# Kernel optimization log

Measured on AMD Instinct MI355X. Metric: run time of the kernel, lower is better.

## Reference

```python
import jax, jax.numpy as jnp
import numpy as np

N_NODES = 50000
N_EDGES = 1_600_000
DIMS = [512, 256, 128]


def _edge_softmax(vals, rows, n):
    # sparse softmax over dim=1 (per source row), only over stored edges
    m = jax.ops.segment_max(vals, rows, num_segments=n)
    e = jnp.exp(vals - m[rows])
    s = jax.ops.segment_sum(e, rows, num_segments=n)
    return e / s[rows]


def _spmm(att, rows, cols, H, n):
    # (sparse C) @ H : gather source cols, scale by edge weight, scatter-add to rows
    return jax.ops.segment_sum(att[:, None] * H[cols], rows, num_segments=n)


def setup_inputs() -> dict:
    key = jax.random.key(0)
    ks = jax.random.split(key, 12)
    X = jax.random.normal(ks[0], (N_NODES, DIMS[0]), dtype=jnp.float32)
    edge_row = jax.random.randint(ks[1], (N_EDGES,), 0, N_NODES, dtype=jnp.int32)
    edge_col = jax.random.randint(ks[2], (N_EDGES,), 0, N_NODES, dtype=jnp.int32)
    A_vals = jnp.ones((N_EDGES,), dtype=jnp.float32)
    def lin(k, dout, din):
        lim = 1.0 / np.sqrt(din)
        return jax.random.uniform(k, (dout, din), jnp.float32, -lim, lim)
    W0 = lin(ks[3], DIMS[1], DIMS[0])
    b0 = jax.random.uniform(ks[4], (DIMS[1],), jnp.float32, -1/np.sqrt(DIMS[0]), 1/np.sqrt(DIMS[0]))
    W1 = lin(ks[5], DIMS[2], DIMS[1])
    b1 = jax.random.uniform(ks[6], (DIMS[2],), jnp.float32, -1/np.sqrt(DIMS[1]), 1/np.sqrt(DIMS[1]))
    v00 = jax.random.normal(ks[7], (DIMS[1],), dtype=jnp.float32)
    v01 = jax.random.normal(ks[8], (DIMS[1],), dtype=jnp.float32)
    v10 = jax.random.normal(ks[9], (DIMS[2],), dtype=jnp.float32)
    v11 = jax.random.normal(ks[10], (DIMS[2],), dtype=jnp.float32)
    return {"X": X, "edge_row": edge_row, "edge_col": edge_col, "A_vals": A_vals,
            "W0": W0, "b0": b0, "W1": W1, "b1": b1,
            "v00": v00, "v01": v01, "v10": v10, "v11": v11}


def reference(X, edge_row, edge_col, A_vals, W0, b0, W1, b1, v00, v01, v10, v11):
    n = X.shape[0]
    layers = [((W0, b0), (v00, v01)), ((W1, b1), (v10, v11))]
    H = X
    atts = []
    # encoder
    for (W, b), (va, vb) in layers:
        M = H @ W.T + b                               # [N, d_out]
        # attention logits are computed under no_grad in the original
        f1 = M @ va                                   # [N]
        f2 = M @ vb
        logits = jax.lax.stop_gradient(A_vals * (f1[edge_row] + f2[edge_col]))
        att = _edge_softmax(jax.nn.sigmoid(logits), edge_row, n)
        H = _spmm(att, edge_row, edge_col, M, n)
        atts.append(att)
    final_H = H
    # decoder (tied weights, reverse order, reuse encoder attention)
    for ((W, _), _), att in zip(reversed(layers), reversed(atts)):
        H = H @ W                                     # F.linear(H, W.t()) == H @ W
        H = _spmm(att, edge_row, edge_col, H, n)
    return H, final_H
```

## Files before the change

### kernel.cpp

```cpp
#include <hip/hip_runtime.h>
#include <cstdint>
#include <cstddef>

typedef __attribute__((ext_vector_type(8))) short bf16x8;
typedef __attribute__((ext_vector_type(4))) float f32x4;

__device__ __forceinline__ ushort f2b(float f) {
    union { float f; uint32_t u; } v; v.f = f;
    uint32_t r = (v.u + 0x7fffu + ((v.u >> 16) & 1u)) >> 16;
    return (ushort)r;
}
__device__ __forceinline__ float b2f(ushort b) {
    union { uint32_t u; float f; } v; v.u = ((uint32_t)b) << 16;
    return v.f;
}


__global__ __launch_bounds__(256) void hist_kernel(const int* __restrict__ rows,
                                                   int* __restrict__ bhist, int E, int nb) {
    __shared__ int h[512];
    for (int i = threadIdx.x; i < nb; i += 256) h[i] = 0;
    __syncthreads();
    int stride = gridDim.x * blockDim.x;
    for (int e = blockIdx.x * blockDim.x + threadIdx.x; e < E; e += stride)
        atomicAdd(&h[rows[e] >> 7], 1);
    __syncthreads();
    for (int i = threadIdx.x; i < nb; i += 256)
        if (h[i]) atomicAdd(&bhist[i], h[i]);
}

__global__ __launch_bounds__(512) void scan512(const int* __restrict__ bhist,
                                               int* __restrict__ boff, int* __restrict__ gcur,
                                               int* __restrict__ rp, int nb, int E, int N) {
    __shared__ int sm[512];
    int v = ((int)threadIdx.x < nb) ? bhist[threadIdx.x] : 0;
    sm[threadIdx.x] = v;
    __syncthreads();
    for (int off = 1; off < 512; off <<= 1) {
        int t = ((int)threadIdx.x >= off) ? sm[threadIdx.x - off] : 0;
        __syncthreads();
        sm[threadIdx.x] += t;
        __syncthreads();
    }
    if ((int)threadIdx.x < nb) {
        int e0 = sm[threadIdx.x] - v;
        boff[threadIdx.x] = e0;
        gcur[threadIdx.x] = e0;
    }
    if (threadIdx.x == 0) { boff[nb] = E; rp[N] = E; }
}

__global__ __launch_bounds__(256) void binpass(const int* __restrict__ rows,
                                               const int* __restrict__ cols,
                                               const float* __restrict__ avals,
                                               int* __restrict__ gcur,
                                               uint2* __restrict__ tmp, int E, int nb) {
    __shared__ int hist[512];
    __shared__ int base[512];
    int e0 = blockIdx.x * 4096;
    int nE = min(4096, E - e0);
    for (int i = threadIdx.x; i < nb; i += 256) hist[i] = 0;
    __syncthreads();
    for (int i = threadIdx.x; i < nE; i += 256)
        atomicAdd(&hist[rows[e0 + i] >> 7], 1);
    __syncthreads();
    for (int i = threadIdx.x; i < nb; i += 256) {
        int c = hist[i];
        if (c) base[i] = atomicAdd(&gcur[i], c);
        hist[i] = 0;
    }
    __syncthreads();
    for (int i = threadIdx.x; i < nE; i += 256) {
        int r = rows[e0 + i];
        int b = r >> 7;
        int loc = atomicAdd(&hist[b], 1);
        uint2 t;
        t.x = ((uint32_t)r << 16) | (uint32_t)cols[e0 + i];
        t.y = __float_as_uint(avals[e0 + i]);
        tmp[base[b] + loc] = t;
    }
}

__global__ __launch_bounds__(256) void bucketpass(const uint2* __restrict__ tmp,
                                                  const int* __restrict__ boff,
                                                  int* __restrict__ rp,
                                                  int* __restrict__ col_s,
                                                  float* __restrict__ a_s, int N) {
    __shared__ int cnt[128];
    __shared__ int pre[128];
    int b = blockIdx.x;
    int r0 = b << 7;
    int nr = min(128, N - r0);
    int t0 = boff[b], t1 = boff[b + 1];
    if ((int)threadIdx.x < 128) cnt[threadIdx.x] = 0;
    __syncthreads();
    for (int i = t0 + (int)threadIdx.x; i < t1; i += 256)
        atomicAdd(&cnt[(tmp[i].x >> 16) - r0], 1);
    __syncthreads();
    if ((int)threadIdx.x < 128) pre[threadIdx.x] = cnt[threadIdx.x];
    __syncthreads();
    for (int off = 1; off < 128; off <<= 1) {
        int t = ((int)threadIdx.x >= off && (int)threadIdx.x < 128) ? pre[threadIdx.x - off] : 0;
        __syncthreads();
        if ((int)threadIdx.x < 128) pre[threadIdx.x] += t;
        __syncthreads();
    }
    if ((int)threadIdx.x < nr) {
        int ex = pre[threadIdx.x] - cnt[threadIdx.x];
        rp[r0 + threadIdx.x] = t0 + ex;
        cnt[threadIdx.x] = t0 + ex;
    }
    __syncthreads();
    for (int i = t0 + (int)threadIdx.x; i < t1; i += 256) {
        uint2 t = tmp[i];
        int lr = (int)(t.x >> 16) - r0;
        int pos = atomicAdd(&cnt[lr], 1);
        col_s[pos] = (int)(t.x & 0xffffu);
        a_s[pos] = __uint_as_float(t.y);
    }
}

__global__ void f2b4_kernel(const float* __restrict__ src, ushort* __restrict__ dst, int n4) {
    int i = blockIdx.x * blockDim.x + threadIdx.x;
    if (i < n4) {
        float4 v = ((const float4*)src)[i];
        ushort4 o;
        o.x = f2b(v.x); o.y = f2b(v.y); o.z = f2b(v.z); o.w = f2b(v.w);
        ((ushort4*)dst)[i] = o;
    }
}

__global__ void transpose_f2b_kernel(const float* __restrict__ W, ushort* __restrict__ Wt,
                                     int rows, int cols) {
    int idx = blockIdx.x * blockDim.x + threadIdx.x;
    if (idx < rows * cols) {
        int r = idx / cols, c = idx % cols;
        Wt[(size_t)c * rows + r] = f2b(W[idx]);
    }
}

__global__ __launch_bounds__(256) void gemm_bf16(const ushort* __restrict__ A,
                                                 const ushort* __restrict__ B,
                                                 const float* __restrict__ bias,
                                                 float* __restrict__ Cf,
                                                 ushort* __restrict__ Ch,
                                                 int M, int K, int Dout) {
    __shared__ ushort As[128][40];
    __shared__ ushort Bs[128][40];
    int bm = blockIdx.y * 128, bn = blockIdx.x * 128;
    int tid = threadIdx.x;
    int w = tid >> 6, l = tid & 63;
    int wm = (w & 1) * 64, wn = (w >> 1) * 64;
    int lm = l & 15, quad = l >> 4;

    f32x4 acc[4][4] = {};

    for (int k0 = 0; k0 < K; k0 += 32) {
#pragma unroll
        for (int it = 0; it < 2; ++it) {
            int L = tid + it * 256;
            int row = L >> 2;
            int ch = (L & 3) * 8;
            int ga = bm + row; if (ga > M - 1) ga = M - 1;
            *(uint4*)&As[row][ch] = *(const uint4*)(A + (size_t)ga * K + k0 + ch);
            *(uint4*)&Bs[row][ch] = *(const uint4*)(B + (size_t)(bn + row) * K + k0 + ch);
        }
        __syncthreads();
        bf16x8 af[4], bfr[4];
#pragma unroll
        for (int i = 0; i < 4; ++i) af[i]  = *(const bf16x8*)&As[wm + i * 16 + lm][quad * 8];
#pragma unroll
        for (int j = 0; j < 4; ++j) bfr[j] = *(const bf16x8*)&Bs[wn + j * 16 + lm][quad * 8];
#pragma unroll
        for (int i = 0; i < 4; ++i)
#pragma unroll
            for (int j = 0; j < 4; ++j)
                acc[i][j] = __builtin_amdgcn_mfma_f32_16x16x32_bf16(af[i], bfr[j], acc[i][j], 0, 0, 0);
        __syncthreads();
    }

    float bv[4] = {0.f, 0.f, 0.f, 0.f};
    if (bias) {
#pragma unroll
        for (int j = 0; j < 4; ++j) bv[j] = bias[bn + wn + j * 16 + lm];
    }
#pragma unroll
    for (int i = 0; i < 4; ++i) {
#pragma unroll
        for (int r = 0; r < 4; ++r) {
            int row = bm + wm + i * 16 + quad * 4 + r;
            if (row < M) {
#pragma unroll
                for (int j = 0; j < 4; ++j) {
                    int col = bn + wn + j * 16 + lm;
                    float v = acc[i][j][r] + bv[j];
                    if (Cf) Cf[(size_t)row * Dout + col] = v;
                    if (Ch) Ch[(size_t)row * Dout + col] = f2b(v);
                }
            }
        }
    }
}

__global__ void fvec_bf16(const ushort* __restrict__ Mh, const float* __restrict__ va,
                          const float* __restrict__ vb, float* __restrict__ f1,
                          float* __restrict__ f2, int d) {
    int n = blockIdx.x;
    int lane = threadIdx.x;
    const ushort* row = Mh + (size_t)n * d;
    float s1 = 0.f, s2 = 0.f;
    for (int k = lane; k < d; k += 64) {
        float m = b2f(row[k]);
        s1 += m * va[k];
        s2 += m * vb[k];
    }
#pragma unroll
    for (int off = 32; off > 0; off >>= 1) {
        s1 += __shfl_xor(s1, off);
        s2 += __shfl_xor(s2, off);
    }
    if (lane == 0) { f1[n] = s1; f2[n] = s2; }
}

__global__ void att_kernel(const int* __restrict__ rp, const int* __restrict__ col_s,
                           const float* __restrict__ a_s, const float* __restrict__ f1,
                           const float* __restrict__ f2, float* __restrict__ att) {
    int r = blockIdx.x;
    int lane = threadIdx.x;
    int beg = rp[r], end = rp[r + 1];
    if (beg == end) return;
    float fr = f1[r];
    float m = -1e30f;
    for (int j = beg + lane; j < end; j += 64) {
        float x = a_s[j] * (fr + f2[col_s[j]]);
        float v = 1.f / (1.f + __expf(-x));
        att[j] = v;
        m = fmaxf(m, v);
    }
#pragma unroll
    for (int off = 32; off > 0; off >>= 1) m = fmaxf(m, __shfl_xor(m, off));
    float s = 0.f;
    for (int j = beg + lane; j < end; j += 64) {
        float e = __expf(att[j] - m);
        att[j] = e;
        s += e;
    }
#pragma unroll
    for (int off = 32; off > 0; off >>= 1) s += __shfl_xor(s, off);
    float inv = 1.f / s;
    for (int j = beg + lane; j < end; j += 64) att[j] *= inv;
}

__global__ __launch_bounds__(256) void spmm_bf16(const int* __restrict__ rp,
                                                 const int* __restrict__ col_s,
                                                 const float* __restrict__ att,
                                                 const ushort* __restrict__ H,
                                                 const float* __restrict__ bias,
                                                 ushort* __restrict__ Oh,
                                                 float* __restrict__ Of,
                                                 int d4, int N) {
    int tid = threadIdx.x;
    int rpb = 256 / d4;
    int r = blockIdx.x * rpb + tid / d4;
    int lane = tid % d4;
    if (r >= N) return;
    int beg = rp[r], end = rp[r + 1];
    float4 acc = make_float4(0.f, 0.f, 0.f, 0.f);
    const ushort4* H4 = (const ushort4*)H;
    int j = beg;
    for (; j + 4 <= end; j += 4) {
        int c0 = col_s[j], c1 = col_s[j + 1], c2 = col_s[j + 2], c3 = col_s[j + 3];
        float w0 = att[j], w1 = att[j + 1], w2 = att[j + 2], w3 = att[j + 3];
        ushort4 h0 = H4[(size_t)c0 * d4 + lane];
        ushort4 h1 = H4[(size_t)c1 * d4 + lane];
        ushort4 h2 = H4[(size_t)c2 * d4 + lane];
        ushort4 h3 = H4[(size_t)c3 * d4 + lane];
        acc.x += w0 * b2f(h0.x) + w1 * b2f(h1.x) + w2 * b2f(h2.x) + w3 * b2f(h3.x);
        acc.y += w0 * b2f(h0.y) + w1 * b2f(h1.y) + w2 * b2f(h2.y) + w3 * b2f(h3.y);
        acc.z += w0 * b2f(h0.z) + w1 * b2f(h1.z) + w2 * b2f(h2.z) + w3 * b2f(h3.z);
        acc.w += w0 * b2f(h0.w) + w1 * b2f(h1.w) + w2 * b2f(h2.w) + w3 * b2f(h3.w);
    }
    for (; j < end; ++j) {
        int c = col_s[j];
        float wgt = att[j];
        ushort4 h = H4[(size_t)c * d4 + lane];
        acc.x += wgt * b2f(h.x);
        acc.y += wgt * b2f(h.y);
        acc.z += wgt * b2f(h.z);
        acc.w += wgt * b2f(h.w);
    }
    if (bias) {
        acc.x += bias[lane * 4 + 0];
        acc.y += bias[lane * 4 + 1];
        acc.z += bias[lane * 4 + 2];
        acc.w += bias[lane * 4 + 3];
    }
    if (Oh) {
        ushort4 o;
        o.x = f2b(acc.x); o.y = f2b(acc.y); o.z = f2b(acc.z); o.w = f2b(acc.w);
        ((ushort4*)Oh)[(size_t)r * d4 + lane] = o;
    }
    if (Of) ((float4*)Of)[(size_t)r * d4 + lane] = acc;
}

extern "C" void kernel_launch(void* const* d_in, const int* in_sizes, int n_in,
                              void* d_out, int out_size, void* d_ws, size_t ws_size,
                              hipStream_t stream) {
    const float* X    = (const float*)d_in[0];
    const int*   erow = (const int*)d_in[1];
    const int*   ecol = (const int*)d_in[2];
    const float* aval = (const float*)d_in[3];
    const float* W0   = (const float*)d_in[4];
    const float* b0   = (const float*)d_in[5];
    const float* W1   = (const float*)d_in[6];
    const float* b1   = (const float*)d_in[7];
    const float* v00  = (const float*)d_in[8];
    const float* v01  = (const float*)d_in[9];
    const float* v10  = (const float*)d_in[10];
    const float* v11  = (const float*)d_in[11];

    const int D0 = 512, D1 = 256, D2 = 128;
    const int N = in_sizes[0] / D0;
    const int E = in_sizes[1];
    const int NB = (N + 127) / 128;
    float* out = (float*)d_out;

    char* ws = (char*)d_ws;
    size_t off = 0;
    auto alloc = [&](size_t bytes) {
        char* p = ws + off;
        off += (bytes + 255) & ~(size_t)255;
        return p;
    };
    ushort* Xh   = (ushort*)alloc((size_t)N * D0 * 2);
    ushort* M0h  = (ushort*)alloc((size_t)N * D1 * 2);
    ushort* Ph   = (ushort*)alloc((size_t)N * D2 * 2);
    ushort* M1h  = (ushort*)alloc((size_t)N * D2 * 2);
    ushort* H2h  = (ushort*)alloc((size_t)N * D2 * 2);
    ushort* S0h  = (ushort*)alloc((size_t)N * D2 * 2);
    ushort* W0h  = (ushort*)alloc((size_t)D1 * D0 * 2);
    ushort* W1h  = (ushort*)alloc((size_t)D2 * D1 * 2);
    ushort* Wt0h = (ushort*)alloc((size_t)D0 * D1 * 2);
    ushort* WfTh = (ushort*)alloc((size_t)D0 * D2 * 2);
    float* att0  = (float*)alloc((size_t)E * 4);
    float* att1  = (float*)alloc((size_t)E * 4);
    float* a_s   = (float*)alloc((size_t)E * 4);
    float* f1    = (float*)alloc((size_t)N * 4);
    float* f2    = (float*)alloc((size_t)N * 4);
    int* rp      = (int*)alloc(((size_t)N + 1) * 4);
    int* col_s   = (int*)alloc((size_t)E * 4);
    uint2* tmp   = (uint2*)alloc((size_t)E * 8);
    int* bhist   = (int*)alloc(512 * 4);
    int* boff    = (int*)alloc(513 * 4);
    int* gcur    = (int*)alloc(512 * 4);

    hipMemsetAsync(bhist, 0, 512 * sizeof(int), stream);
    hist_kernel<<<256, 256, 0, stream>>>(erow, bhist, E, NB);
    scan512<<<1, 512, 0, stream>>>(bhist, boff, gcur, rp, NB, E, N);
    binpass<<<(E + 4095) / 4096, 256, 0, stream>>>(erow, ecol, aval, gcur, tmp, E, NB);
    bucketpass<<<NB, 256, 0, stream>>>(tmp, boff, rp, col_s, a_s, N);

    f2b4_kernel<<<((N * D0 / 4) + 255) / 256, 256, 0, stream>>>(X, Xh, N * D0 / 4);
    f2b4_kernel<<<((D1 * D0 / 4) + 255) / 256, 256, 0, stream>>>(W0, W0h, D1 * D0 / 4);
    f2b4_kernel<<<((D2 * D1 / 4) + 255) / 256, 256, 0, stream>>>(W1, W1h, D2 * D1 / 4);
    transpose_f2b_kernel<<<(D1 * D0 + 255) / 256, 256, 0, stream>>>(W0, Wt0h, D1, D0);

    gemm_bf16<<<dim3(1, 4), 256, 0, stream>>>(Wt0h, W1h, nullptr, nullptr, WfTh, D0, D1, D2);

    const int gy = (N + 127) / 128;
    const int sgrid = (N + 7) / 8;

    gemm_bf16<<<dim3(D1 / 128, gy), 256, 0, stream>>>(Xh, W0h, b0, nullptr, M0h, N, D0, D1);
    fvec_bf16<<<N, 64, 0, stream>>>(M0h, v00, v01, f1, f2, D1);
    att_kernel<<<N, 64, 0, stream>>>(rp, col_s, a_s, f1, f2, att0);
    gemm_bf16<<<dim3(1, gy), 256, 0, stream>>>(M0h, W1h, nullptr, nullptr, Ph, N, D1, D2);
    spmm_bf16<<<sgrid, 256, 0, stream>>>(rp, col_s, att0, Ph, b1, M1h, nullptr, D2 / 4, N);
    fvec_bf16<<<N, 64, 0, stream>>>(M1h, v10, v11, f1, f2, D2);
    att_kernel<<<N, 64, 0, stream>>>(rp, col_s, a_s, f1, f2, att1);
    spmm_bf16<<<sgrid, 256, 0, stream>>>(rp, col_s, att1, M1h, nullptr, H2h,
                                         out + (size_t)N * D0, D2 / 4, N);

    spmm_bf16<<<sgrid, 256, 0, stream>>>(rp, col_s, att1, H2h, nullptr, Ph, nullptr, D2 / 4, N);
    spmm_bf16<<<sgrid, 256, 0, stream>>>(rp, col_s, att0, Ph, nullptr, S0h, nullptr, D2 / 4, N);
    gemm_bf16<<<dim3(D0 / 128, gy), 256, 0, stream>>>(S0h, WfTh, nullptr, out, nullptr, N, D2, D0);
}
```

Measured before the change: 694.1 us.

## Rework GEMM with direct-to-LDS swizzled loads and fuse attention/SpMM epilogues

The GEMM now stages 64-wide K tiles through global_load_lds with an XOR swizzle, which removes the register round trip and avoids LDS bank conflicts. Edge softmax drops the max pass and the normalise pass: sigmoid outputs lie in (0,1), so exp is safe without a max, and the per-row reciprocal is applied inside the SpMM. The second layer's attention dot products (f1/f2) are computed in the first SpMM's epilogue, which removes one fvec kernel and one full read of M1. The SpMM uses 16 lanes per row with 16-byte loads, and the weight prep kernels are merged into one launch. All of this specialises the code to fixed dimensions (256 and 128).

```diff
diff --git a/kernel.cpp b/kernel.cpp
--- a/kernel.cpp
+++ b/kernel.cpp
@@ -15,6 +15,10 @@
     return v.f;
 }
 
+__device__ __forceinline__ void gll16(const void* g, void* l) {
+    __builtin_amdgcn_global_load_lds((const __attribute__((address_space(1))) void*)g,
+                                     (__attribute__((address_space(3))) void*)l, 16, 0, 0);
+}
 
 __global__ __launch_bounds__(256) void hist_kernel(const int* __restrict__ rows,
                                                    int* __restrict__ bhist, int E, int nb) {
@@ -130,12 +134,27 @@
     }
 }
 
-__global__ void transpose_f2b_kernel(const float* __restrict__ W, ushort* __restrict__ Wt,
-                                     int rows, int cols) {
-    int idx = blockIdx.x * blockDim.x + threadIdx.x;
-    if (idx < rows * cols) {
-        int r = idx / cols, c = idx % cols;
-        Wt[(size_t)c * rows + r] = f2b(W[idx]);
+__global__ __launch_bounds__(256) void prep_weights(const float* __restrict__ W0,
+                                                    const float* __restrict__ W1,
+                                                    ushort* __restrict__ W0h,
+                                                    ushort* __restrict__ W1h,
+                                                    ushort* __restrict__ Wt0h) {
+    int i = blockIdx.x * 256 + threadIdx.x;
+    float4 v = ((const float4*)W0)[i];
+    ushort4 o;
+    o.x = f2b(v.x); o.y = f2b(v.y); o.z = f2b(v.z); o.w = f2b(v.w);
+    ((ushort4*)W0h)[i] = o;
+    int r = (i * 4) >> 9;
+    int c = (i * 4) & 511;
+    Wt0h[(size_t)(c + 0) * 256 + r] = o.x;
+    Wt0h[(size_t)(c + 1) * 256 + r] = o.y;
+    Wt0h[(size_t)(c + 2) * 256 + r] = o.z;
+    Wt0h[(size_t)(c + 3) * 256 + r] = o.w;
+    if (i < 8192) {
+        float4 w = ((const float4*)W1)[i];
+        ushort4 p;
+        p.x = f2b(w.x); p.y = f2b(w.y); p.z = f2b(w.z); p.w = f2b(w.w);
+        ((ushort4*)W1h)[i] = p;
     }
 }
 
@@ -145,37 +164,47 @@
                                                  float* __restrict__ Cf,
                                                  ushort* __restrict__ Ch,
                                                  int M, int K, int Dout) {
-    __shared__ ushort As[128][40];
-    __shared__ ushort Bs[128][40];
+    __shared__ ushort As[128 * 64];
+    __shared__ ushort Bs[128 * 64];
     int bm = blockIdx.y * 128, bn = blockIdx.x * 128;
     int tid = threadIdx.x;
     int w = tid >> 6, l = tid & 63;
     int wm = (w & 1) * 64, wn = (w >> 1) * 64;
     int lm = l & 15, quad = l >> 4;
+    int wslot = tid & 192;
 
     f32x4 acc[4][4] = {};
 
-    for (int k0 = 0; k0 < K; k0 += 32) {
-#pragma unroll
-        for (int it = 0; it < 2; ++it) {
-            int L = tid + it * 256;
-            int row = L >> 2;
-            int ch = (L & 3) * 8;
+    for (int k0 = 0; k0 < K; k0 += 64) {
+#pragma unroll
+        for (int it = 0; it < 4; ++it) {
+            int slot = it * 256 + tid;
+            int row = slot >> 3;
+            int qg = ((slot & 7) ^ (row & 7)) * 8;
             int ga = bm + row; if (ga > M - 1) ga = M - 1;
-            *(uint4*)&As[row][ch] = *(const uint4*)(A + (size_t)ga * K + k0 + ch);
-            *(uint4*)&Bs[row][ch] = *(const uint4*)(B + (size_t)(bn + row) * K + k0 + ch);
+            gll16(A + (size_t)ga * K + k0 + qg, As + (size_t)(it * 256 + wslot) * 8);
+            gll16(B + (size_t)(bn + row) * K + k0 + qg, Bs + (size_t)(it * 256 + wslot) * 8);
         }
         __syncthreads();
-        bf16x8 af[4], bfr[4];
-#pragma unroll
-        for (int i = 0; i < 4; ++i) af[i]  = *(const bf16x8*)&As[wm + i * 16 + lm][quad * 8];
-#pragma unroll
-        for (int j = 0; j < 4; ++j) bfr[j] = *(const bf16x8*)&Bs[wn + j * 16 + lm][quad * 8];
-#pragma unroll
-        for (int i = 0; i < 4; ++i)
-#pragma unroll
-            for (int j = 0; j < 4; ++j)
-                acc[i][j] = __builtin_amdgcn_mfma_f32_16x16x32_bf16(af[i], bfr[j], acc[i][j], 0, 0, 0);
+#pragma unroll
+        for (int ks = 0; ks < 2; ++ks) {
+            bf16x8 af[4], bfr[4];
+#pragma unroll
+            for (int i = 0; i < 4; ++i) {
+                int r = wm + i * 16 + lm;
+                af[i] = *(const bf16x8*)&As[r * 64 + (((ks * 4 + quad) ^ (r & 7)) * 8)];
+            }
+#pragma unroll
+            for (int j = 0; j < 4; ++j) {
+                int r = wn + j * 16 + lm;
+                bfr[j] = *(const bf16x8*)&Bs[r * 64 + (((ks * 4 + quad) ^ (r & 7)) * 8)];
+            }
+#pragma unroll
+            for (int i = 0; i < 4; ++i)
+#pragma unroll
+                for (int j = 0; j < 4; ++j)
+                    acc[i][j] = __builtin_amdgcn_mfma_f32_16x16x32_bf16(af[i], bfr[j], acc[i][j], 0, 0, 0);
+        }
         __syncthreads();
     }
 
@@ -202,18 +231,20 @@
     }
 }
 
-__global__ void fvec_bf16(const ushort* __restrict__ Mh, const float* __restrict__ va,
-                          const float* __restrict__ vb, float* __restrict__ f1,
-                          float* __restrict__ f2, int d) {
-    int n = blockIdx.x;
-    int lane = threadIdx.x;
-    const ushort* row = Mh + (size_t)n * d;
-    float s1 = 0.f, s2 = 0.f;
-    for (int k = lane; k < d; k += 64) {
-        float m = b2f(row[k]);
-        s1 += m * va[k];
-        s2 += m * vb[k];
-    }
+__global__ __launch_bounds__(256) void fvec256_kernel(const ushort* __restrict__ Mh,
+                                                      const float* __restrict__ va,
+                                                      const float* __restrict__ vb,
+                                                      float* __restrict__ f1,
+                                                      float* __restrict__ f2, int N) {
+    int n = blockIdx.x * 4 + (threadIdx.x >> 6);
+    if (n >= N) return;
+    int lane = threadIdx.x & 63;
+    ushort4 m4 = ((const ushort4*)(Mh + (size_t)n * 256))[lane];
+    float4 a4 = ((const float4*)va)[lane];
+    float4 b4 = ((const float4*)vb)[lane];
+    float m0 = b2f(m4.x), m1 = b2f(m4.y), m2 = b2f(m4.z), m3 = b2f(m4.w);
+    float s1 = m0 * a4.x + m1 * a4.y + m2 * a4.z + m3 * a4.w;
+    float s2 = m0 * b4.x + m1 * b4.y + m2 * b4.z + m3 * b4.w;
 #pragma unroll
     for (int off = 32; off > 0; off >>= 1) {
         s1 += __shfl_xor(s1, off);
@@ -222,85 +253,111 @@
     if (lane == 0) { f1[n] = s1; f2[n] = s2; }
 }
 
-__global__ void att_kernel(const int* __restrict__ rp, const int* __restrict__ col_s,
-                           const float* __restrict__ a_s, const float* __restrict__ f1,
-                           const float* __restrict__ f2, float* __restrict__ att) {
-    int r = blockIdx.x;
-    int lane = threadIdx.x;
+__global__ __launch_bounds__(256) void att2_kernel(const int* __restrict__ rp,
+                                                   const int* __restrict__ col_s,
+                                                   const float* __restrict__ a_s,
+                                                   const float* __restrict__ f1,
+                                                   const float* __restrict__ f2,
+                                                   float* __restrict__ att,
+                                                   float* __restrict__ rs, int N) {
+    int r = blockIdx.x * 4 + (threadIdx.x >> 6);
+    if (r >= N) return;
+    int lane = threadIdx.x & 63;
     int beg = rp[r], end = rp[r + 1];
-    if (beg == end) return;
     float fr = f1[r];
-    float m = -1e30f;
+    float s = 0.f;
     for (int j = beg + lane; j < end; j += 64) {
         float x = a_s[j] * (fr + f2[col_s[j]]);
         float v = 1.f / (1.f + __expf(-x));
-        att[j] = v;
-        m = fmaxf(m, v);
-    }
-#pragma unroll
-    for (int off = 32; off > 0; off >>= 1) m = fmaxf(m, __shfl_xor(m, off));
-    float s = 0.f;
-    for (int j = beg + lane; j < end; j += 64) {
-        float e = __expf(att[j] - m);
+        float e = __expf(v);
         att[j] = e;
         s += e;
     }
 #pragma unroll
     for (int off = 32; off > 0; off >>= 1) s += __shfl_xor(s, off);
-    float inv = 1.f / s;
-    for (int j = beg + lane; j < end; j += 64) att[j] *= inv;
-}
-
-__global__ __launch_bounds__(256) void spmm_bf16(const int* __restrict__ rp,
-                                                 const int* __restrict__ col_s,
-                                                 const float* __restrict__ att,
-                                                 const ushort* __restrict__ H,
-                                                 const float* __restrict__ bias,
-                                                 ushort* __restrict__ Oh,
-                                                 float* __restrict__ Of,
-                                                 int d4, int N) {
-    int tid = threadIdx.x;
-    int rpb = 256 / d4;
-    int r = blockIdx.x * rpb + tid / d4;
-    int lane = tid % d4;
+    if (lane == 0) rs[r] = (end > beg) ? 1.f / s : 0.f;
+}
+
+__global__ __launch_bounds__(256) void spmm128(const int* __restrict__ rp,
+                                               const int* __restrict__ col_s,
+                                               const float* __restrict__ att,
+                                               const float* __restrict__ rs,
+                                               const ushort* __restrict__ H,
+                                               const float* __restrict__ bias,
+                                               const float* __restrict__ va,
+                                               const float* __restrict__ vb,
+                                               float* __restrict__ f1,
+                                               float* __restrict__ f2,
+                                               ushort* __restrict__ Oh,
+                                               float* __restrict__ Of, int N) {
+    int r = blockIdx.x * 16 + (threadIdx.x >> 4);
     if (r >= N) return;
+    int lane = threadIdx.x & 15;
     int beg = rp[r], end = rp[r + 1];
-    float4 acc = make_float4(0.f, 0.f, 0.f, 0.f);
-    const ushort4* H4 = (const ushort4*)H;
+    float acc[8] = {0.f, 0.f, 0.f, 0.f, 0.f, 0.f, 0.f, 0.f};
+    const uint4* H4 = (const uint4*)H;
+#define FMA8(h, wgt) { \
+        acc[0] += (wgt) * b2f((ushort)((h).x & 0xffffu)); \
+        acc[1] += (wgt) * b2f((ushort)((h).x >> 16)); \
+        acc[2] += (wgt) * b2f((ushort)((h).y & 0xffffu)); \
+        acc[3] += (wgt) * b2f((ushort)((h).y >> 16)); \
+        acc[4] += (wgt) * b2f((ushort)((h).z & 0xffffu)); \
+        acc[5] += (wgt) * b2f((ushort)((h).z >> 16)); \
+        acc[6] += (wgt) * b2f((ushort)((h).w & 0xffffu)); \
+        acc[7] += (wgt) * b2f((ushort)((h).w >> 16)); }
     int j = beg;
     for (; j + 4 <= end; j += 4) {
         int c0 = col_s[j], c1 = col_s[j + 1], c2 = col_s[j + 2], c3 = col_s[j + 3];
         float w0 = att[j], w1 = att[j + 1], w2 = att[j + 2], w3 = att[j + 3];
-        ushort4 h0 = H4[(size_t)c0 * d4 + lane];
-        ushort4 h1 = H4[(size_t)c1 * d4 + lane];
-        ushort4 h2 = H4[(size_t)c2 * d4 + lane];
-        ushort4 h3 = H4[(size_t)c3 * d4 + lane];
-        acc.x += w0 * b2f(h0.x) + w1 * b2f(h1.x) + w2 * b2f(h2.x) + w3 * b2f(h3.x);
-        acc.y += w0 * b2f(h0.y) + w1 * b2f(h1.y) + w2 * b2f(h2.y) + w3 * b2f(h3.y);
-        acc.z += w0 * b2f(h0.z) + w1 * b2f(h1.z) + w2 * b2f(h2.z) + w3 * b2f(h3.z);
-        acc.w += w0 * b2f(h0.w) + w1 * b2f(h1.w) + w2 * b2f(h2.w) + w3 * b2f(h3.w);
+        uint4 h0 = H4[(size_t)c0 * 16 + lane];
+        uint4 h1 = H4[(size_t)c1 * 16 + lane];
+        uint4 h2 = H4[(size_t)c2 * 16 + lane];
+        uint4 h3 = H4[(size_t)c3 * 16 + lane];
+        FMA8(h0, w0) FMA8(h1, w1) FMA8(h2, w2) FMA8(h3, w3)
     }
     for (; j < end; ++j) {
-        int c = col_s[j];
-        float wgt = att[j];
-        ushort4 h = H4[(size_t)c * d4 + lane];
-        acc.x += wgt * b2f(h.x);
-        acc.y += wgt * b2f(h.y);
-        acc.z += wgt * b2f(h.z);
-        acc.w += wgt * b2f(h.w);
-    }
+        uint4 h = H4[(size_t)col_s[j] * 16 + lane];
+        float w0 = att[j];
+        FMA8(h, w0)
+    }
+#undef FMA8
+    float rsv = rs[r];
+#pragma unroll
+    for (int k = 0; k < 8; ++k) acc[k] *= rsv;
     if (bias) {
-        acc.x += bias[lane * 4 + 0];
-        acc.y += bias[lane * 4 + 1];
-        acc.z += bias[lane * 4 + 2];
-        acc.w += bias[lane * 4 + 3];
+        const float4* b4 = (const float4*)(bias + lane * 8);
+        float4 ba = b4[0], bb = b4[1];
+        acc[0] += ba.x; acc[1] += ba.y; acc[2] += ba.z; acc[3] += ba.w;
+        acc[4] += bb.x; acc[5] += bb.y; acc[6] += bb.z; acc[7] += bb.w;
+    }
+    if (va) {
+        const float4* a4 = (const float4*)(va + lane * 8);
+        const float4* c4 = (const float4*)(vb + lane * 8);
+        float4 va0 = a4[0], va1 = a4[1], vb0 = c4[0], vb1 = c4[1];
+        float p1 = acc[0] * va0.x + acc[1] * va0.y + acc[2] * va0.z + acc[3] * va0.w
+                 + acc[4] * va1.x + acc[5] * va1.y + acc[6] * va1.z + acc[7] * va1.w;
+        float p2 = acc[0] * vb0.x + acc[1] * vb0.y + acc[2] * vb0.z + acc[3] * vb0.w
+                 + acc[4] * vb1.x + acc[5] * vb1.y + acc[6] * vb1.z + acc[7] * vb1.w;
+#pragma unroll
+        for (int off = 8; off > 0; off >>= 1) {
+            p1 += __shfl_xor(p1, off);
+            p2 += __shfl_xor(p2, off);
+        }
+        if (lane == 0) { f1[r] = p1; f2[r] = p2; }
     }
     if (Oh) {
-        ushort4 o;
-        o.x = f2b(acc.x); o.y = f2b(acc.y); o.z = f2b(acc.z); o.w = f2b(acc.w);
-        ((ushort4*)Oh)[(size_t)r * d4 + lane] = o;
-    }
-    if (Of) ((float4*)Of)[(size_t)r * d4 + lane] = acc;
+        uint4 o;
+        o.x = (uint32_t)f2b(acc[0]) | ((uint32_t)f2b(acc[1]) << 16);
+        o.y = (uint32_t)f2b(acc[2]) | ((uint32_t)f2b(acc[3]) << 16);
+        o.z = (uint32_t)f2b(acc[4]) | ((uint32_t)f2b(acc[5]) << 16);
+        o.w = (uint32_t)f2b(acc[6]) | ((uint32_t)f2b(acc[7]) << 16);
+        ((uint4*)Oh)[(size_t)r * 16 + lane] = o;
+    }
+    if (Of) {
+        float4* O4 = (float4*)Of;
+        O4[(size_t)r * 32 + lane * 2]     = make_float4(acc[0], acc[1], acc[2], acc[3]);
+        O4[(size_t)r * 32 + lane * 2 + 1] = make_float4(acc[4], acc[5], acc[6], acc[7]);
+    }
 }
 
 extern "C" void kernel_launch(void* const* d_in, const int* in_sizes, int n_in,
@@ -347,6 +404,8 @@
     float* a_s   = (float*)alloc((size_t)E * 4);
     float* f1    = (float*)alloc((size_t)N * 4);
     float* f2    = (float*)alloc((size_t)N * 4);
+    float* rs0   = (float*)alloc((size_t)N * 4);
+    float* rs1   = (float*)alloc((size_t)N * 4);
     int* rp      = (int*)alloc(((size_t)N + 1) * 4);
     int* col_s   = (int*)alloc((size_t)E * 4);
     uint2* tmp   = (uint2*)alloc((size_t)E * 8);
@@ -361,26 +420,30 @@
     bucketpass<<<NB, 256, 0, stream>>>(tmp, boff, rp, col_s, a_s, N);
 
     f2b4_kernel<<<((N * D0 / 4) + 255) / 256, 256, 0, stream>>>(X, Xh, N * D0 / 4);
-    f2b4_kernel<<<((D1 * D0 / 4) + 255) / 256, 256, 0, stream>>>(W0, W0h, D1 * D0 / 4);
-    f2b4_kernel<<<((D2 * D1 / 4) + 255) / 256, 256, 0, stream>>>(W1, W1h, D2 * D1 / 4);
-    transpose_f2b_kernel<<<(D1 * D0 + 255) / 256, 256, 0, stream>>>(W0, Wt0h, D1, D0);
+    prep_weights<<<128, 256, 0, stream>>>(W0, W1, W0h, W1h, Wt0h);
 
     gemm_bf16<<<dim3(1, 4), 256, 0, stream>>>(Wt0h, W1h, nullptr, nullptr, WfTh, D0, D1, D2);
 
     const int gy = (N + 127) / 128;
-    const int sgrid = (N + 7) / 8;
+    const int agrid = (N + 3) / 4;
+    const int sgrid = (N + 15) / 16;
 
     gemm_bf16<<<dim3(D1 / 128, gy), 256, 0, stream>>>(Xh, W0h, b0, nullptr, M0h, N, D0, D1);
-    fvec_bf16<<<N, 64, 0, stream>>>(M0h, v00, v01, f1, f2, D1);
-    att_kernel<<<N, 64, 0, stream>>>(rp, col_s, a_s, f1, f2, att0);
+    fvec256_kernel<<<agrid, 256, 0, stream>>>(M0h, v00, v01, f1, f2, N);
+    att2_kernel<<<agrid, 256, 0, stream>>>(rp, col_s, a_s, f1, f2, att0, rs0, N);
     gemm_bf16<<<dim3(1, gy), 256, 0, stream>>>(M0h, W1h, nullptr, nullptr, Ph, N, D1, D2);
-    spmm_bf16<<<sgrid, 256, 0, stream>>>(rp, col_s, att0, Ph, b1, M1h, nullptr, D2 / 4, N);
-    fvec_bf16<<<N, 64, 0, stream>>>(M1h, v10, v11, f1, f2, D2);
-    att_kernel<<<N, 64, 0, stream>>>(rp, col_s, a_s, f1, f2, att1);
-    spmm_bf16<<<sgrid, 256, 0, stream>>>(rp, col_s, att1, M1h, nullptr, H2h,
-                                         out + (size_t)N * D0, D2 / 4, N);
-
-    spmm_bf16<<<sgrid, 256, 0, stream>>>(rp, col_s, att1, H2h, nullptr, Ph, nullptr, D2 / 4, N);
-    spmm_bf16<<<sgrid, 256, 0, stream>>>(rp, col_s, att0, Ph, nullptr, S0h, nullptr, D2 / 4, N);
+    spmm128<<<sgrid, 256, 0, stream>>>(rp, col_s, att0, rs0, Ph, b1, v10, v11, f1, f2,
+                                       M1h, nullptr, N);
+    att2_kernel<<<agrid, 256, 0, stream>>>(rp, col_s, a_s, f1, f2, att1, rs1, N);
+    spmm128<<<sgrid, 256, 0, stream>>>(rp, col_s, att1, rs1, M1h, nullptr,
+                                       nullptr, nullptr, nullptr, nullptr,
+                                       H2h, out + (size_t)N * D0, N);
+
+    spmm128<<<sgrid, 256, 0, stream>>>(rp, col_s, att1, rs1, H2h, nullptr,
+                                       nullptr, nullptr, nullptr, nullptr,
+                                       Ph, nullptr, N);
+    spmm128<<<sgrid, 256, 0, stream>>>(rp, col_s, att0, rs0, Ph, nullptr,
+                                       nullptr, nullptr, nullptr, nullptr,
+                                       S0h, nullptr, N);
     gemm_bf16<<<dim3(D0 / 128, gy), 256, 0, stream>>>(S0h, WfTh, nullptr, out, nullptr, N, D2, D0);
 }
```

After: 655.8 us. -5.5%, faster.
